# Optimization experiments

Hardware: AMD Instinct MI355X
Metric: run time of the kernel (lower is better)

## Reference

```python
import jax, jax.numpy as jnp
import numpy as np

EMBED_DIM = 1024
NUM_HEADS = 16
HEAD_DIM = EMBED_DIM // NUM_HEADS


def setup_inputs() -> dict:
    key = jax.random.key(0)
    ks = jax.random.split(key, 9)
    s = 1.0 / np.sqrt(EMBED_DIM)
    X = jax.random.normal(ks[0], (4, 2048, EMBED_DIM), dtype=jnp.float32)
    # Linear weights stored as [in, out] for x @ W + b
    Wq = jax.random.uniform(ks[1], (EMBED_DIM, EMBED_DIM), jnp.float32, -s, s)
    bq = jax.random.uniform(ks[2], (EMBED_DIM,), jnp.float32, -s, s)
    Wk = jax.random.uniform(ks[3], (EMBED_DIM, EMBED_DIM), jnp.float32, -s, s)
    bk = jax.random.uniform(ks[4], (EMBED_DIM,), jnp.float32, -s, s)
    Wv = jax.random.uniform(ks[5], (EMBED_DIM, EMBED_DIM), jnp.float32, -s, s)
    bv = jax.random.uniform(ks[6], (EMBED_DIM,), jnp.float32, -s, s)
    Wo = jax.random.uniform(ks[7], (EMBED_DIM, EMBED_DIM), jnp.float32, -s, s)
    bo = jax.random.uniform(ks[8], (EMBED_DIM,), jnp.float32, -s, s)
    return {"X": X, "Wq": Wq, "bq": bq, "Wk": Wk, "bk": bk,
            "Wv": Wv, "bv": bv, "Wo": Wo, "bo": bo}


def reference(X, Wq, bq, Wk, bk, Wv, bv, Wo, bo):
    B, S, _ = X.shape
    def split_heads(t):  # [B,S,E] -> [B,H,S,D]
        return t.reshape(B, S, NUM_HEADS, HEAD_DIM).transpose(0, 2, 1, 3)
    Q = split_heads(X @ Wq + bq)
    K = split_heads(X @ Wk + bk)
    V = split_heads(X @ Wv + bv)
    scale = 1.0 / np.sqrt(HEAD_DIM).astype(np.float32)
    scores = jnp.einsum('bhqd,bhkd->bhqk', Q, K) * scale
    probs = jax.nn.softmax(scores, axis=-1)
    attn = jnp.einsum('bhqk,bhkd->bhqd', probs, V)  # [B,H,S,D]
    combined = attn.transpose(0, 2, 1, 3).reshape(B, S, EMBED_DIM)
    return combined @ Wo + bo
```

## Files before the change

### kernel.cpp

```cpp
#include <hip/hip_runtime.h>
#include <hip/hip_bf16.h>

#define EMBED 1024
#define NHEADS 16
#define HDIM 64
#define SEQ 2048
#define BATCH 4
#define ROWS (BATCH * SEQ)

typedef __attribute__((ext_vector_type(8))) short bf16x8;
typedef __attribute__((ext_vector_type(4))) float f32x4;
typedef __attribute__((ext_vector_type(2))) float f32x2;
typedef __attribute__((ext_vector_type(16))) float f32x16;
typedef __attribute__((ext_vector_type(4))) unsigned int u32x4;
typedef __attribute__((ext_vector_type(2))) unsigned int u32x2;
typedef __attribute__((ext_vector_type(2))) int i32x2;
typedef unsigned int u32;

#define SL2E 0.18033688011112042f

__device__ __forceinline__ short f2bf(float f) {
    u32 u = __builtin_bit_cast(u32, f) + 0x8000u;
    return (short)(u >> 16);
}

__device__ __forceinline__ u32 pkbf(float a, float b) {
    u32 ua = __builtin_bit_cast(u32, a) + 0x8000u;
    u32 ub = __builtin_bit_cast(u32, b) + 0x8000u;
    return __builtin_amdgcn_perm(ua, ub, 0x03020706u);
}

__device__ __forceinline__ float fexp2(float x) {
#if __has_builtin(__builtin_amdgcn_exp2f)
    return __builtin_amdgcn_exp2f(x);
#else
    return exp2f(x);
#endif
}

__device__ __forceinline__ void async16(const void* g, void* l) {
    __builtin_amdgcn_global_load_lds((const __attribute__((address_space(1))) u32*)g,
                                     (__attribute__((address_space(3))) u32*)l, 16, 0, 0);
}

__global__ __launch_bounds__(256) void convert_f32_bf16(const float* __restrict__ in,
                                                        short* __restrict__ out) {
    int i = (blockIdx.x * 256 + threadIdx.x) * 4;
    float4 v = *(const float4*)&in[i];
    u32x2 o = { pkbf(v.x, v.y), pkbf(v.z, v.w) };
    *(u32x2*)&out[i] = o;
}

__global__ __launch_bounds__(256) void transpose_w4(const float* __restrict__ W0,
                                                    const float* __restrict__ W1,
                                                    const float* __restrict__ W2,
                                                    const float* __restrict__ W3,
                                                    short* __restrict__ T0,
                                                    short* __restrict__ T1,
                                                    short* __restrict__ T2,
                                                    short* __restrict__ T3) {
    const int z = blockIdx.z;
    const float* W = (z == 0) ? W0 : (z == 1) ? W1 : (z == 2) ? W2 : W3;
    short* WT = (z == 0) ? T0 : (z == 1) ? T1 : (z == 2) ? T2 : T3;
    const float sc = (z == 0) ? SL2E : 1.0f;
    __shared__ float T[64][65];
    const int k0 = blockIdx.y * 64, n0 = blockIdx.x * 64;
    const int rr = threadIdx.x >> 4, cc = (threadIdx.x & 15) * 4;
    #pragma unroll
    for (int p = 0; p < 4; ++p) {
        int r = p * 16 + rr;
        float4 v = *(const float4*)&W[(size_t)(k0 + r) * EMBED + n0 + cc];
        T[r][cc] = v.x * sc; T[r][cc + 1] = v.y * sc; T[r][cc + 2] = v.z * sc; T[r][cc + 3] = v.w * sc;
    }
    __syncthreads();
    #pragma unroll
    for (int p = 0; p < 4; ++p) {
        int r = p * 16 + rr;
        u32x2 o = { pkbf(T[cc][r], T[cc + 1][r]), pkbf(T[cc + 2][r], T[cc + 3][r]) };
        *(u32x2*)&WT[(size_t)(n0 + r) * EMBED + k0 + cc] = o;
    }
}

__global__ __launch_bounds__(512, 2) void gemm_p128(const short* __restrict__ A,
                                                    const short* __restrict__ BT,
                                                    const float* __restrict__ b0,
                                                    const float* __restrict__ b1,
                                                    const float* __restrict__ b2,
                                                    void* __restrict__ C0,
                                                    void* __restrict__ C1,
                                                    void* __restrict__ C2,
                                                    int mode) {
    __shared__ short As[2][8192];
    __shared__ short Bs[2][16384];
    const int tid = threadIdx.x;
    const int lane = tid & 63;
    const int wid = tid >> 6;
    const int c16 = lane & 15, quad = lane >> 4, sw = c16 & 7;
    const int wm = wid >> 2, wn = wid & 3;
    const int gx = gridDim.x;
    const int hid = blockIdx.y * gx + blockIdx.x;
    const int cpx = (gx * gridDim.y) >> 3;
    const int tle = (hid & 7) * cpx + (hid >> 3);
    const int bx = tle % gx, by = tle / gx;
    const int rowblk = by * 128, colblk = bx * 256;

    const int r0 = tid >> 3;
    const int g0 = (tid & 7) ^ (r0 & 7);
    const short* aS0 = A + (size_t)(rowblk + r0) * EMBED + g0 * 8;
    const short* bS0 = BT + (size_t)(colblk + r0) * EMBED + g0 * 8;

#define STAGE_A(SBUF, V) do { \
    const short* _s = aS0 + (V) * 64; \
    async16(_s,         &As[SBUF][tid * 8]); \
    async16(_s + 65536, &As[SBUF][tid * 8 + 4096]); \
} while (0)
#define STAGE_B0(SBUF, V) do { \
    const short* _s = bS0 + (V) * 64; \
    async16(_s,         &Bs[SBUF][tid * 8]); \
    async16(_s + 65536, &Bs[SBUF][tid * 8 + 4096]); \
} while (0)
#define STAGE_B1(SBUF, V) do { \
    const short* _s = bS0 + 131072 + (V) * 64; \
    async16(_s,         &Bs[SBUF][tid * 8 + 8192]); \
    async16(_s + 65536, &Bs[SBUF][tid * 8 + 12288]); \
} while (0)

    f32x4 acc[4][4] = {};
    bf16x8 aU[2][2], bE[2][2], bO[2][2];

#define LDA(BUF, MH) do { \
    _Pragma("unroll") \
    for (int fm = 0; fm < 2; ++fm) { \
        const int row = wm * 64 + (MH) * 32 + fm * 16 + c16; \
        _Pragma("unroll") \
        for (int ks = 0; ks < 2; ++ks) \
            aU[fm][ks] = *(const bf16x8*)&As[BUF][row * 64 + ((ks * 4 + quad) ^ sw) * 8]; \
    } \
} while (0)
#define LDB(BUF, NH, DST) do { \
    _Pragma("unroll") \
    for (int fn = 0; fn < 2; ++fn) { \
        const int col = wn * 64 + (NH) * 32 + fn * 16 + c16; \
        _Pragma("unroll") \
        for (int ks = 0; ks < 2; ++ks) \
            DST[fn][ks] = *(const bf16x8*)&Bs[BUF][col * 64 + ((ks * 4 + quad) ^ sw) * 8]; \
    } \
} while (0)
#define MM(MB, NB, BM_) do { \
    _Pragma("unroll") \
    for (int fm = 0; fm < 2; ++fm) \
        _Pragma("unroll") \
        for (int fn = 0; fn < 2; ++fn) \
            _Pragma("unroll") \
            for (int ks = 0; ks < 2; ++ks) \
                acc[(MB) + fm][(NB) + fn] = \
                    __builtin_amdgcn_mfma_f32_16x16x32_bf16(aU[fm][ks], BM_[fn][ks], \
                        acc[(MB) + fm][(NB) + fn], 0, 0, 0); \
} while (0)
#define PH_MID() do { \
    __builtin_amdgcn_s_barrier(); \
    asm volatile("s_waitcnt lgkmcnt(0)" ::: "memory"); \
    __builtin_amdgcn_s_setprio(1); \
} while (0)
#define PH_END(VM) do { \
    __builtin_amdgcn_s_setprio(0); \
    if (VM) asm volatile("s_waitcnt vmcnt(6)" ::: "memory"); \
    __builtin_amdgcn_s_barrier(); \
} while (0)

    STAGE_B0(0, 0); STAGE_A(0, 0); STAGE_B1(0, 0);
    STAGE_B0(1, 1); STAGE_A(1, 1); STAGE_B1(1, 1);
    asm volatile("s_waitcnt vmcnt(6)" ::: "memory");
    __builtin_amdgcn_s_barrier();

    #pragma unroll 1
    for (int it = 0; it < 8; ++it) {
        const int u = 2 * it;
        const int v2 = (u + 2) & 15, v3 = (u + 3) & 15;
        LDA(0, 0); LDB(0, 0, bE);                     PH_MID(); MM(0, 0, bE); PH_END(0);
        LDB(0, 1, bO);            STAGE_B0(0, v2);    PH_MID(); MM(0, 2, bO); PH_END(0);
        LDA(0, 1);                STAGE_B1(0, v2);    PH_MID(); MM(2, 2, bO); PH_END(0);
                 STAGE_A(0, v2);     PH_MID(); MM(2, 0, bE); PH_END(1);
        LDA(1, 0); LDB(1, 0, bE);                     PH_MID(); MM(0, 0, bE); PH_END(0);
        LDB(1, 1, bO);            STAGE_B0(1, v3);    PH_MID(); MM(0, 2, bO); PH_END(0);
        LDA(1, 1);                STAGE_B1(1, v3);    PH_MID(); MM(2, 2, bO); PH_END(0);
                 STAGE_A(1, v3);     PH_MID(); MM(2, 0, bE); PH_END(1);
    }

    asm volatile("s_waitcnt vmcnt(0)" ::: "memory");

    const int rb0 = rowblk + wm * 64 + quad * 4;
    const int cb0 = wn * 64 + c16;
    if (mode == 0) {
        const int z = colblk >> 10;
        const int cm = colblk & 1023;
        const float* bias = (z == 0) ? b0 : (z == 1) ? b1 : b2;
        if (z == 2) {
            short* Vt = (short*)C2;
            #pragma unroll
            for (int m = 0; m < 4; ++m) {
                const int row = rb0 + (m >> 1) * 32 + (m & 1) * 16;
                const int b = row >> 11, s = row & 2047;
                #pragma unroll
                for (int n = 0; n < 4; ++n) {
                    const int cv = cm + cb0 + (n >> 1) * 32 + (n & 1) * 16;
                    const int head = cv >> 6, d = cv & 63;
                    const float bv = bias[cv];
                    u32x2 o = { pkbf(acc[m][n][0] + bv, acc[m][n][1] + bv),
                                pkbf(acc[m][n][2] + bv, acc[m][n][3] + bv) };
                    *(u32x2*)&Vt[((size_t)(b * NHEADS + head) * HDIM + d) * SEQ + s] = o;
                }
            }
        } else {
            short* Cq = (short*)((z == 0) ? C0 : C1);
            const float bsc = (z == 0) ? SL2E : 1.0f;
            #pragma unroll
            for (int m = 0; m < 4; ++m) {
                const int row = rb0 + (m >> 1) * 32 + (m & 1) * 16;
                #pragma unroll
                for (int n = 0; n < 4; ++n) {
                    const int col = cm + cb0 + (n >> 1) * 32 + (n & 1) * 16;
                    const float bv = bias[col] * bsc;
                    #pragma unroll
                    for (int r = 0; r < 4; ++r)
                        Cq[(size_t)(row + r) * EMBED + col] = f2bf(acc[m][n][r] + bv);
                }
            }
        }
    } else {
        float* Co = (float*)C0;
        #pragma unroll
        for (int m = 0; m < 4; ++m) {
            const int row = rb0 + (m >> 1) * 32 + (m & 1) * 16;
            #pragma unroll
            for (int n = 0; n < 4; ++n) {
                const int col = colblk + cb0 + (n >> 1) * 32 + (n & 1) * 16;
                const float bv = b0[col];
                #pragma unroll
                for (int r = 0; r < 4; ++r)
                    Co[(size_t)(row + r) * EMBED + col] = acc[m][n][r] + bv;
            }
        }
    }
#undef PH_END
#undef PH_MID
#undef MM
#undef LDB
#undef LDA
#undef STAGE_B1
#undef STAGE_B0
#undef STAGE_A
}

__global__ __launch_bounds__(256, 4) void attn_mfma(const short* __restrict__ Qb,
                                                    const short* __restrict__ Kb,
                                                    const short* __restrict__ Vt,
                                                    short* __restrict__ Ob) {
    __shared__ short SH[16384];
    const int tid = threadIdx.x;
    const int wave = tid >> 6, lane = tid & 63;
    const int l31 = lane & 31, h = lane >> 5;
    const int swz = l31 & 7;
    const int hid = blockIdx.y * 16 + blockIdx.x;
    const int tle = (hid & 7) * 128 + (hid >> 3);
    const int qb = tle & 15, bh = tle >> 4;
    const int b = bh >> 4, hd = bh & 15;
    const size_t base = (size_t)b * SEQ * EMBED + (size_t)hd * HDIM;
    const size_t vbase = (size_t)bh * HDIM * SEQ;
    const int q0 = qb * 128;

    bf16x8 qf[4];
    #pragma unroll
    for (int ks = 0; ks < 4; ++ks)
        qf[ks] = *(const bf16x8*)&Qb[base + (size_t)(q0 + wave * 32 + l31) * EMBED + ks * 16 + h * 8];

    const short* kp[2];
    const short* vp[2];
    int ldofs[2];
    #pragma unroll
    for (int it = 0; it < 2; ++it) {
        int ci = (it * 4 + wave) * 64 + lane;
        int row = ci >> 3, g = (ci & 7) ^ (row & 7);
        kp[it] = Kb + base + (size_t)row * EMBED + g * 8;
        vp[it] = Vt + vbase + (size_t)row * SEQ + g * 8;
        ldofs[it] = (it * 4 + wave) * 512;
    }

#define STAGE_KV(J) do { \
    async16(kp[0], &SH[(J) * 4096 + ldofs[0]]); \
    async16(kp[1], &SH[(J) * 4096 + ldofs[1]]); \
    async16(vp[0], &SH[8192 + (J) * 4096 + ldofs[0]]); \
    async16(vp[1], &SH[8192 + (J) * 4096 + ldofs[1]]); \
    kp[0] += 64 * EMBED; kp[1] += 64 * EMBED; \
    vp[0] += 64; vp[1] += 64; \
} while (0)

    f32x16 O[2] = {};
    f32x2 ls = {0.0f, 0.0f};

    STAGE_KV(0);
    asm volatile("s_waitcnt vmcnt(0)" ::: "memory");
    __builtin_amdgcn_s_barrier();

#define ATT_TILE(CUR, NXT, DO_STAGE) do { \
    if (DO_STAGE) STAGE_KV(NXT); \
    _Pragma("unroll") \
    for (int nt = 0; nt < 2; ++nt) { \
        f32x16 st = {0.0f, 0.0f, 0.0f, 0.0f, 0.0f, 0.0f, 0.0f, 0.0f, \
                     0.0f, 0.0f, 0.0f, 0.0f, 0.0f, 0.0f, 0.0f, 0.0f}; \
        __builtin_amdgcn_s_setprio(1); \
        _Pragma("unroll") \
        for (int ks = 0; ks < 4; ++ks) { \
            bf16x8 ak = *(const bf16x8*)&SH[(CUR) * 4096 + (nt * 32 + l31) * 64 + ((ks * 2 + h) ^ swz) * 8]; \
            st = __builtin_amdgcn_mfma_f32_32x32x16_bf16(ak, qf[ks], st, 0, 0, 0); \
        } \
        __builtin_amdgcn_s_setprio(0); \
        u32 pk[8]; \
        _Pragma("unroll") \
        for (int i = 0; i < 8; ++i) { \
            float e0 = fexp2(st[2 * i]), e1 = fexp2(st[2 * i + 1]); \
            f32x2 e = { e0, e1 }; \
            ls += e; \
            pk[i] = pkbf(e0, e1); \
        } \
        __builtin_amdgcn_s_setprio(1); \
        _Pragma("unroll") \
        for (int kk = 0; kk < 2; ++kk) { \
            const int ks = nt * 2 + kk, bs = kk * 4; \
            u32x4 fr; \
            i32x2 sA = __builtin_amdgcn_permlane32_swap((int)pk[bs + 0], (int)pk[bs + 2], false, false); \
            i32x2 sB = __builtin_amdgcn_permlane32_swap((int)pk[bs + 1], (int)pk[bs + 3], false, false); \
            fr.x = (u32)sA.x; fr.y = (u32)sB.x; fr.z = (u32)sA.y; fr.w = (u32)sB.y; \
            bf16x8 pf = __builtin_bit_cast(bf16x8, fr); \
            _Pragma("unroll") \
            for (int mt = 0; mt < 2; ++mt) { \
                bf16x8 vf = *(const bf16x8*)&SH[8192 + (CUR) * 4096 + (mt * 32 + l31) * 64 + ((ks * 2 + h) ^ swz) * 8]; \
                O[mt] = __builtin_amdgcn_mfma_f32_32x32x16_bf16(vf, pf, O[mt], 0, 0, 0); \
            } \
        } \
        __builtin_amdgcn_s_setprio(0); \
    } \
    asm volatile("s_waitcnt vmcnt(0)" ::: "memory"); \
    __builtin_amdgcn_s_barrier(); \
} while (0)

    #pragma unroll 1
    for (int t = 0; t < 30; t += 2) {
        ATT_TILE(0, 1, 1);
        ATT_TILE(1, 0, 1);
    }
    ATT_TILE(0, 1, 1);
    ATT_TILE(1, 0, 0);

#undef ATT_TILE
#undef STAGE_KV

    float lsum = ls.x + ls.y;
    lsum += __shfl_xor(lsum, 32);
    float inv = 1.0f / lsum;

    const int wbase = wave * 2048;
    #pragma unroll
    for (int mt = 0; mt < 2; ++mt)
        #pragma unroll
        for (int m = 0; m < 4; ++m) {
            u32x2 wv;
            wv.x = pkbf(O[mt][4 * m + 0] * inv, O[mt][4 * m + 1] * inv);
            wv.y = pkbf(O[mt][4 * m + 2] * inv, O[mt][4 * m + 3] * inv);
            int u = mt * 8 + 2 * m + h;
            int su = u ^ ((l31 & 7) << 1);
            *(u32x2*)&SH[wbase + l31 * 64 + su * 4] = wv;
        }
    __syncthreads();
    #pragma unroll
    for (int p = 0; p < 4; ++p) {
        int ci = p * 256 + tid;
        int wq = ci >> 8, rem = ci & 255;
        int r = rem >> 3, cch = rem & 7;
        int su = (2 * cch) ^ ((r & 7) << 1);
        bf16x8 val = *(const bf16x8*)&SH[wq * 2048 + r * 64 + su * 4];
        *(bf16x8*)&Ob[base + (size_t)(q0 + wq * 32 + r) * EMBED + cch * 8] = val;
    }
}

extern "C" void kernel_launch(void* const* d_in, const int* in_sizes, int n_in,
                              void* d_out, int out_size, void* d_ws, size_t ws_size,
                              hipStream_t stream)
{
    const float* X  = (const float*)d_in[0];
    const float* Wq = (const float*)d_in[1];
    const float* bq = (const float*)d_in[2];
    const float* Wk = (const float*)d_in[3];
    const float* bk = (const float*)d_in[4];
    const float* Wv = (const float*)d_in[5];
    const float* bv = (const float*)d_in[6];
    const float* Wo = (const float*)d_in[7];
    const float* bo = (const float*)d_in[8];
    float* out = (float*)d_out;

    const size_t NE = (size_t)ROWS * EMBED;
    short* Xbf = (short*)d_ws;
    short* Qb  = Xbf + NE;
    short* Kb  = Qb + NE;
    short* Vtb = Kb + NE;
    short* WqT = Vtb + NE;
    short* WkT = WqT + (size_t)EMBED * EMBED;
    short* WvT = WkT + (size_t)EMBED * EMBED;
    short* WoT = WvT + (size_t)EMBED * EMBED;

    convert_f32_bf16<<<(ROWS * EMBED) / 1024, 256, 0, stream>>>(X, Xbf);
    dim3 gw(16, 16, 4);
    transpose_w4<<<gw, 256, 0, stream>>>(Wq, Wk, Wv, Wo, WqT, WkT, WvT, WoT);

    dim3 gq(12, 64, 1);
    gemm_p128<<<gq, 512, 0, stream>>>(Xbf, WqT, bq, bk, bv, Qb, Kb, Vtb, 0);

    dim3 gt(SEQ / 128, BATCH * NHEADS);
    attn_mfma<<<gt, 256, 0, stream>>>(Qb, Kb, Vtb, Qb);

    dim3 gg(4, 64, 1);
    gemm_p128<<<gg, 512, 0, stream>>>(Qb, WoT, bo, bo, bo, out, out, out, 1);
}
```

Measured before the change: 259.4 us.

## Replace pipelined 128x256 GEMM with simple 128x128 single-buffer kernel; use hardware bf16 pack

```diff
diff --git a/kernel.cpp b/kernel.cpp
--- a/kernel.cpp
+++ b/kernel.cpp
@@ -28,6 +28,12 @@
     u32 ua = __builtin_bit_cast(u32, a) + 0x8000u;
     u32 ub = __builtin_bit_cast(u32, b) + 0x8000u;
     return __builtin_amdgcn_perm(ua, ub, 0x03020706u);
+}
+
+__device__ __forceinline__ u32 cvtpk(float a, float b) {
+    u32 r;
+    asm("v_cvt_pk_bf16_f32 %0, %1, %2" : "=v"(r) : "v"(a), "v"(b));
+    return r;
 }
 
 __device__ __forceinline__ float fexp2(float x) {
@@ -81,113 +87,62 @@
     }
 }
 
-__global__ __launch_bounds__(512, 2) void gemm_p128(const short* __restrict__ A,
-                                                    const short* __restrict__ BT,
-                                                    const float* __restrict__ b0,
-                                                    const float* __restrict__ b1,
-                                                    const float* __restrict__ b2,
-                                                    void* __restrict__ C0,
-                                                    void* __restrict__ C1,
-                                                    void* __restrict__ C2,
-                                                    int mode) {
-    __shared__ short As[2][8192];
-    __shared__ short Bs[2][16384];
+__global__ __launch_bounds__(256, 4) void gemm_sq128(const short* __restrict__ A,
+                                                     const short* __restrict__ BT,
+                                                     const float* __restrict__ b0,
+                                                     const float* __restrict__ b1,
+                                                     const float* __restrict__ b2,
+                                                     void* __restrict__ C0,
+                                                     void* __restrict__ C1,
+                                                     void* __restrict__ C2,
+                                                     int mode) {
+    __shared__ short As[128 * 64];
+    __shared__ short Bs[128 * 64];
     const int tid = threadIdx.x;
     const int lane = tid & 63;
     const int wid = tid >> 6;
     const int c16 = lane & 15, quad = lane >> 4, sw = c16 & 7;
-    const int wm = wid >> 2, wn = wid & 3;
+    const int wm = wid >> 1, wn = wid & 1;
     const int gx = gridDim.x;
     const int hid = blockIdx.y * gx + blockIdx.x;
     const int cpx = (gx * gridDim.y) >> 3;
     const int tle = (hid & 7) * cpx + (hid >> 3);
     const int bx = tle % gx, by = tle / gx;
-    const int rowblk = by * 128, colblk = bx * 256;
+    const int rowblk = by * 128, colblk = bx * 128;
 
     const int r0 = tid >> 3;
     const int g0 = (tid & 7) ^ (r0 & 7);
-    const short* aS0 = A + (size_t)(rowblk + r0) * EMBED + g0 * 8;
-    const short* bS0 = BT + (size_t)(colblk + r0) * EMBED + g0 * 8;
-
-#define STAGE_A(SBUF, V) do { \
-    const short* _s = aS0 + (V) * 64; \
-    async16(_s,         &As[SBUF][tid * 8]); \
-    async16(_s + 65536, &As[SBUF][tid * 8 + 4096]); \
-} while (0)
-#define STAGE_B0(SBUF, V) do { \
-    const short* _s = bS0 + (V) * 64; \
-    async16(_s,         &Bs[SBUF][tid * 8]); \
-    async16(_s + 65536, &Bs[SBUF][tid * 8 + 4096]); \
-} while (0)
-#define STAGE_B1(SBUF, V) do { \
-    const short* _s = bS0 + 131072 + (V) * 64; \
-    async16(_s,         &Bs[SBUF][tid * 8 + 8192]); \
-    async16(_s + 65536, &Bs[SBUF][tid * 8 + 12288]); \
-} while (0)
+    const short* aS = A + (size_t)(rowblk + r0) * EMBED + g0 * 8;
+    const short* bS = BT + (size_t)(colblk + r0) * EMBED + g0 * 8;
 
     f32x4 acc[4][4] = {};
-    bf16x8 aU[2][2], bE[2][2], bO[2][2];
-
-#define LDA(BUF, MH) do { \
-    _Pragma("unroll") \
-    for (int fm = 0; fm < 2; ++fm) { \
-        const int row = wm * 64 + (MH) * 32 + fm * 16 + c16; \
-        _Pragma("unroll") \
-        for (int ks = 0; ks < 2; ++ks) \
-            aU[fm][ks] = *(const bf16x8*)&As[BUF][row * 64 + ((ks * 4 + quad) ^ sw) * 8]; \
-    } \
-} while (0)
-#define LDB(BUF, NH, DST) do { \
-    _Pragma("unroll") \
-    for (int fn = 0; fn < 2; ++fn) { \
-        const int col = wn * 64 + (NH) * 32 + fn * 16 + c16; \
-        _Pragma("unroll") \
-        for (int ks = 0; ks < 2; ++ks) \
-            DST[fn][ks] = *(const bf16x8*)&Bs[BUF][col * 64 + ((ks * 4 + quad) ^ sw) * 8]; \
-    } \
-} while (0)
-#define MM(MB, NB, BM_) do { \
-    _Pragma("unroll") \
-    for (int fm = 0; fm < 2; ++fm) \
-        _Pragma("unroll") \
-        for (int fn = 0; fn < 2; ++fn) \
-            _Pragma("unroll") \
-            for (int ks = 0; ks < 2; ++ks) \
-                acc[(MB) + fm][(NB) + fn] = \
-                    __builtin_amdgcn_mfma_f32_16x16x32_bf16(aU[fm][ks], BM_[fn][ks], \
-                        acc[(MB) + fm][(NB) + fn], 0, 0, 0); \
-} while (0)
-#define PH_MID() do { \
-    __builtin_amdgcn_s_barrier(); \
-    asm volatile("s_waitcnt lgkmcnt(0)" ::: "memory"); \
-    __builtin_amdgcn_s_setprio(1); \
-} while (0)
-#define PH_END(VM) do { \
-    __builtin_amdgcn_s_setprio(0); \
-    if (VM) asm volatile("s_waitcnt vmcnt(6)" ::: "memory"); \
-    __builtin_amdgcn_s_barrier(); \
-} while (0)
-
-    STAGE_B0(0, 0); STAGE_A(0, 0); STAGE_B1(0, 0);
-    STAGE_B0(1, 1); STAGE_A(1, 1); STAGE_B1(1, 1);
-    asm volatile("s_waitcnt vmcnt(6)" ::: "memory");
-    __builtin_amdgcn_s_barrier();
 
     #pragma unroll 1
-    for (int it = 0; it < 8; ++it) {
-        const int u = 2 * it;
-        const int v2 = (u + 2) & 15, v3 = (u + 3) & 15;
-        LDA(0, 0); LDB(0, 0, bE);                     PH_MID(); MM(0, 0, bE); PH_END(0);
-        LDB(0, 1, bO);            STAGE_B0(0, v2);    PH_MID(); MM(0, 2, bO); PH_END(0);
-        LDA(0, 1);                STAGE_B1(0, v2);    PH_MID(); MM(2, 2, bO); PH_END(0);
-                 STAGE_A(0, v2);     PH_MID(); MM(2, 0, bE); PH_END(1);
-        LDA(1, 0); LDB(1, 0, bE);                     PH_MID(); MM(0, 0, bE); PH_END(0);
-        LDB(1, 1, bO);            STAGE_B0(1, v3);    PH_MID(); MM(0, 2, bO); PH_END(0);
-        LDA(1, 1);                STAGE_B1(1, v3);    PH_MID(); MM(2, 2, bO); PH_END(0);
-                 STAGE_A(1, v3);     PH_MID(); MM(2, 0, bE); PH_END(1);
-    }
-
-    asm volatile("s_waitcnt vmcnt(0)" ::: "memory");
+    for (int k0 = 0; k0 < EMBED; k0 += 64) {
+        #pragma unroll
+        for (int p = 0; p < 4; ++p)
+            async16(aS + p * (32 * EMBED) + k0, &As[tid * 8 + p * 2048]);
+        #pragma unroll
+        for (int p = 0; p < 4; ++p)
+            async16(bS + p * (32 * EMBED) + k0, &Bs[tid * 8 + p * 2048]);
+        __syncthreads();
+        #pragma unroll
+        for (int ks = 0; ks < 2; ++ks) {
+            bf16x8 af[4], bfr[4];
+            #pragma unroll
+            for (int fm = 0; fm < 4; ++fm)
+                af[fm] = *(const bf16x8*)&As[(wm * 64 + fm * 16 + c16) * 64 + ((ks * 4 + quad) ^ sw) * 8];
+            #pragma unroll
+            for (int fn = 0; fn < 4; ++fn)
+                bfr[fn] = *(const bf16x8*)&Bs[(wn * 64 + fn * 16 + c16) * 64 + ((ks * 4 + quad) ^ sw) * 8];
+            #pragma unroll
+            for (int fm = 0; fm < 4; ++fm)
+                #pragma unroll
+                for (int fn = 0; fn < 4; ++fn)
+                    acc[fm][fn] = __builtin_amdgcn_mfma_f32_16x16x32_bf16(af[fm], bfr[fn], acc[fm][fn], 0, 0, 0);
+        }
+        __syncthreads();
+    }
 
     const int rb0 = rowblk + wm * 64 + quad * 4;
     const int cb0 = wn * 64 + c16;
@@ -198,16 +153,16 @@
         if (z == 2) {
             short* Vt = (short*)C2;
             #pragma unroll
-            for (int m = 0; m < 4; ++m) {
-                const int row = rb0 + (m >> 1) * 32 + (m & 1) * 16;
+            for (int fm = 0; fm < 4; ++fm) {
+                const int row = rb0 + fm * 16;
                 const int b = row >> 11, s = row & 2047;
                 #pragma unroll
-                for (int n = 0; n < 4; ++n) {
-                    const int cv = cm + cb0 + (n >> 1) * 32 + (n & 1) * 16;
+                for (int fn = 0; fn < 4; ++fn) {
+                    const int cv = cm + cb0 + fn * 16;
                     const int head = cv >> 6, d = cv & 63;
                     const float bv = bias[cv];
-                    u32x2 o = { pkbf(acc[m][n][0] + bv, acc[m][n][1] + bv),
-                                pkbf(acc[m][n][2] + bv, acc[m][n][3] + bv) };
+                    u32x2 o = { pkbf(acc[fm][fn][0] + bv, acc[fm][fn][1] + bv),
+                                pkbf(acc[fm][fn][2] + bv, acc[fm][fn][3] + bv) };
                     *(u32x2*)&Vt[((size_t)(b * NHEADS + head) * HDIM + d) * SEQ + s] = o;
                 }
             }
@@ -215,41 +170,33 @@
             short* Cq = (short*)((z == 0) ? C0 : C1);
             const float bsc = (z == 0) ? SL2E : 1.0f;
             #pragma unroll
-            for (int m = 0; m < 4; ++m) {
-                const int row = rb0 + (m >> 1) * 32 + (m & 1) * 16;
+            for (int fm = 0; fm < 4; ++fm) {
+                const int row = rb0 + fm * 16;
                 #pragma unroll
-                for (int n = 0; n < 4; ++n) {
-                    const int col = cm + cb0 + (n >> 1) * 32 + (n & 1) * 16;
+                for (int fn = 0; fn < 4; ++fn) {
+                    const int col = cm + cb0 + fn * 16;
                     const float bv = bias[col] * bsc;
                     #pragma unroll
                     for (int r = 0; r < 4; ++r)
-                        Cq[(size_t)(row + r) * EMBED + col] = f2bf(acc[m][n][r] + bv);
+                        Cq[(size_t)(row + r) * EMBED + col] = f2bf(acc[fm][fn][r] + bv);
                 }
             }
         }
     } else {
         float* Co = (float*)C0;
         #pragma unroll
-        for (int m = 0; m < 4; ++m) {
-            const int row = rb0 + (m >> 1) * 32 + (m & 1) * 16;
-            #pragma unroll
-            for (int n = 0; n < 4; ++n) {
-                const int col = colblk + cb0 + (n >> 1) * 32 + (n & 1) * 16;
+        for (int fm = 0; fm < 4; ++fm) {
+            const int row = rb0 + fm * 16;
+            #pragma unroll
+            for (int fn = 0; fn < 4; ++fn) {
+                const int col = colblk + cb0 + fn * 16;
                 const float bv = b0[col];
                 #pragma unroll
                 for (int r = 0; r < 4; ++r)
-                    Co[(size_t)(row + r) * EMBED + col] = acc[m][n][r] + bv;
+                    Co[(size_t)(row + r) * EMBED + col] = acc[fm][fn][r] + bv;
             }
         }
     }
-#undef PH_END
-#undef PH_MID
-#undef MM
-#undef LDB
-#undef LDA
-#undef STAGE_B1
-#undef STAGE_B0
-#undef STAGE_A
 }
 
 __global__ __launch_bounds__(256, 4) void attn_mfma(const short* __restrict__ Qb,
@@ -321,7 +268,7 @@
             float e0 = fexp2(st[2 * i]), e1 = fexp2(st[2 * i + 1]); \
             f32x2 e = { e0, e1 }; \
             ls += e; \
-            pk[i] = pkbf(e0, e1); \
+            pk[i] = cvtpk(e0, e1); \
         } \
         __builtin_amdgcn_s_setprio(1); \
         _Pragma("unroll") \
@@ -412,12 +359,12 @@
     dim3 gw(16, 16, 4);
     transpose_w4<<<gw, 256, 0, stream>>>(Wq, Wk, Wv, Wo, WqT, WkT, WvT, WoT);
 
-    dim3 gq(12, 64, 1);
-    gemm_p128<<<gq, 512, 0, stream>>>(Xbf, WqT, bq, bk, bv, Qb, Kb, Vtb, 0);
+    dim3 gq(24, 64, 1);
+    gemm_sq128<<<gq, 256, 0, stream>>>(Xbf, WqT, bq, bk, bv, Qb, Kb, Vtb, 0);
 
     dim3 gt(SEQ / 128, BATCH * NHEADS);
     attn_mfma<<<gt, 256, 0, stream>>>(Qb, Kb, Vtb, Qb);
 
-    dim3 gg(4, 64, 1);
-    gemm_p128<<<gg, 512, 0, stream>>>(Qb, WoT, bo, bo, bo, out, out, out, 1);
-}
+    dim3 gg(8, 64, 1);
+    gemm_sq128<<<gg, 256, 0, stream>>>(Qb, WoT, bo, bo, bo, out, out, out, 1);
+}
```

After: 260.0 us. No clear change (+0.3%).
